# Kernel tuning notes

Measured on AMD Instinct MI355X. Metric: run time of the kernel, lower is better.

Reference implementation:

```python
import jax, jax.numpy as jnp
import numpy as np

G, N_REAL, C_IN, C_EDGE, H, D, C_EOUT = 4096, 31, 64, 64, 4, 64, 64
N_NODE = N_REAL + 1  # 32, last local node is the supernode


def setup_inputs() -> dict:
    key = jax.random.key(0)
    # per-graph edge template: bidirectional ring over real nodes (consecutive (u,v),(v,u) pairs),
    # then edges (u, supernode)
    u = np.arange(N_REAL)
    v = (u + 1) % N_REAL
    ring_src = np.stack([u, v], 1).reshape(-1)
    ring_dst = np.stack([v, u], 1).reshape(-1)
    ls = np.concatenate([ring_src, np.arange(N_REAL)])
    ld = np.concatenate([ring_dst, np.full(N_REAL, N_REAL)])
    Eg = ls.shape[0]  # 93
    off = np.arange(G) * N_NODE
    edge_index = np.stack([(off[:, None] + ls[None, :]).reshape(-1),
                           (off[:, None] + ld[None, :]).reshape(-1)])
    N = G * N_NODE
    E = G * Eg
    k1, k2, k3, k4, k5 = jax.random.split(key, 5)
    return {
        "x": jax.random.normal(k1, (N, C_IN), jnp.float32),
        "edge_index": jnp.asarray(edge_index, jnp.int32),
        "edge_inform": jax.random.normal(k2, (E, C_EDGE), jnp.float32) * 0.1,
        "batch": jnp.asarray(np.repeat(np.arange(G), N_NODE), jnp.int32),
        "edge_num": jnp.asarray(np.full(G, Eg), jnp.int32),
        "W_lin_l": jax.random.normal(k3, (C_IN + C_EDGE, H * D), jnp.float32) * 0.05,
        "att_l": jax.random.normal(k4, (1, H, D), jnp.float32) * 0.1,
        "bias": jnp.zeros((D,), jnp.float32),
        "W_ec": jax.random.normal(k5, (C_EDGE, C_EOUT), jnp.float32) * 0.1,
        "b_ec": jnp.zeros((C_EOUT,), jnp.float32),
    }


def reference(x, edge_index, edge_inform, batch, edge_num, W_lin_l, att_l, bias, W_ec, b_ec):
    # graph structure is static metadata -> numpy
    ei = np.asarray(edge_index)
    en = np.asarray(edge_num)
    N = x.shape[0]
    G_ = en.shape[0]
    Eg = int(en[0])
    n = N // G_
    src = jnp.asarray(ei[0])
    dst = jnp.asarray(ei[1])
    Hh, Dd = att_l.shape[1], att_l.shape[2]

    # degree counting (the per-edge python loop in the original)
    deg = jnp.zeros((N,), x.dtype).at[dst].add(1.0)

    # GAT-style edge attention + scatter-sum
    h = jnp.concatenate([x[src], edge_inform], axis=1) @ W_lin_l  # [E, H*D]
    h = h.reshape(-1, Hh, Dd)
    alpha = jax.nn.leaky_relu(jnp.sum(h * att_l, axis=-1))  # [E,H], slope 0.01
    amax = jax.ops.segment_max(alpha, dst, num_segments=N)
    ex = jnp.exp(alpha - amax[dst])
    a = ex / (jax.ops.segment_sum(ex, dst, num_segments=N)[dst] + 1e-16)
    xi = jax.ops.segment_sum(h * a[..., None], dst, num_segments=N)  # [N,H,D]
    out = xi.mean(axis=1) + bias

    # per-graph edge aggregation (structure uniform across graphs by construction)
    le = ei.reshape(2, G_, Eg) - (np.arange(G_) * n)[None, :, None]
    l0, l1 = le[0, 0], le[1, 0]  # local template indices, same for every graph
    midx = np.nonzero((l1 != n - 1) & (l0 != l1))[0]  # mask: drop supernode-dst & self-loops
    even = midx[0::2]
    C = edge_inform.shape[1]
    inf_g = edge_inform.reshape(G_, Eg, C)

    mdst = jnp.asarray(l1[midx])
    eisum = jax.vmap(lambda v: jax.ops.segment_sum(v, mdst, num_segments=n - 1))(inf_g[:, midx])  # [G,n-1,C]

    es, ed = l0[even], l1[even]
    deg_g = deg.reshape(G_, n)
    norm = deg_g[:, es] + deg_g[:, ed] - 2.0  # edge_norm; divide by edge_norm - 1
    temp = (eisum[:, es] + eisum[:, ed] - inf_g[:, even]) / (norm - 1.0)[..., None]  # [G,P,C]
    temps2 = jnp.repeat(temp, 2, axis=1)  # each temp appended twice

    l1_all = jnp.asarray(l1)
    cnt = jnp.zeros((n,), x.dtype).at[l1_all].add(1.0)
    esum_all = jax.vmap(lambda v: jax.ops.segment_sum(v, l1_all, num_segments=n))(inf_g)
    emean = esum_all / cnt[None, :, None]  # scatter reduce='mean'

    gather = jnp.concatenate([temps2, emean, emean[:, : n - 1]], axis=1).reshape(-1, C)
    new_edge_inform = jax.nn.leaky_relu(gather @ W_ec + b_ec)
    return out, new_edge_inform
```

## Files before the change

kernel.cpp:

```cpp
#include <hip/hip_runtime.h>
#include <hip/hip_fp16.h>

#define NUM_G 4096
#define RS 72
#define OUT2_OFF ((size_t)NUM_G * 32 * 64)

typedef _Float16 half8  __attribute__((ext_vector_type(8)));
typedef _Float16 half4v __attribute__((ext_vector_type(4)));
typedef _Float16 half2v __attribute__((ext_vector_type(2)));
typedef float    floatx4 __attribute__((ext_vector_type(4)));

__device__ __forceinline__ float lrelu(float v) { return v > 0.f ? v : 0.01f * v; }

__global__ void setup_prep(const float* __restrict__ W, const float* __restrict__ att,
                           const float* __restrict__ Wec,
                           _Float16* __restrict__ vp, _Float16* __restrict__ BT,
                           _Float16* __restrict__ BT2)
{
    const int t = threadIdx.x, b = blockIdx.x;
    if (b == 0) {
        for (int i = t; i < 512; i += 256) {
            const int h8 = i >> 6, k = i & 63;
            const int h = h8 & 3, ro = (h8 < 4) ? 0 : 64;
            float acc = 0.f;
            for (int d = 0; d < 64; ++d) acc += W[(ro + k) * 256 + h * 64 + d] * att[h * 64 + d];
            vp[i] = (_Float16)acc;
        }
    }
    for (int i = b * 4096 + t; i < (b + 1) * 4096; i += 256) {
        const int d = i >> 9, kk = i & 511, h = kk >> 7, k = kk & 127;
        BT[i] = (_Float16)W[k * 256 + h * 64 + d];
    }
    for (int i = b * 512 + t; i < b * 512 + 512; i += 256) {
        const int d = i >> 6, k = i & 63;
        BT2[i] = (_Float16)Wec[k * 64 + d];
    }
}

__global__ __launch_bounds__(256, 4) void fused_main(
    const float* __restrict__ x, const float* __restrict__ einf,
    const float* __restrict__ bias, const float* __restrict__ bec,
    const _Float16* __restrict__ vp, const _Float16* __restrict__ BT,
    const _Float16* __restrict__ BT2,
    float* __restrict__ out, float* __restrict__ out2)
{
    __shared__ __align__(16) _Float16 R[128 * RS];
    __shared__ __align__(16) unsigned char U[9216];
    _Float16* vpl  = (_Float16*)U;
    float*    sal  = (float*)(U + 1152);
    _Float16* virt = (_Float16*)(U + 5760);
    float*    al4  = (float*)(U + 6784);
    _Float16* A2   = (_Float16*)U;

    const int t = threadIdx.x;
    const int g = blockIdx.x;
    const int lane = t & 63;
    const int w = t >> 6;
    const int m16 = lane & 15, q = lane >> 4;

    {
        const float4* xg4 = (const float4*)(x + (size_t)g * 2048);
        for (int i = t; i < 512; i += 256) {
            float4 v = xg4[i];
            half4v h4 = {(_Float16)v.x, (_Float16)v.y, (_Float16)v.z, (_Float16)v.w};
            *(half4v*)(R + (i >> 4) * RS + (i & 15) * 4) = h4;
        }
        const float4* eg4 = (const float4*)(einf + (size_t)g * 5952);
        for (int i = t; i < 1488; i += 256) {
            float4 v = eg4[i];
            half4v h4 = {(_Float16)v.x, (_Float16)v.y, (_Float16)v.z, (_Float16)v.w};
            *(half4v*)(R + (32 + (i >> 4)) * RS + (i & 15) * 4) = h4;
        }
        for (int i = t; i < 512; i += 256)
            vpl[(i >> 6) * RS + (i & 63)] = vp[i];
    }
    __syncthreads();

    #pragma unroll
    for (int j = 0; j < 4; ++j) {
        const int combo = t + 256 * j;
        const int r = combo >> 3, h8 = combo & 7;
        const _Float16* rr = R + r * RS;
        const _Float16* vr = vpl + h8 * RS;
        half8 a8 = {0, 0, 0, 0, 0, 0, 0, 0};
        #pragma unroll
        for (int k8 = 0; k8 < 8; ++k8)
            a8 += (*(const half8*)(rr + k8 * 8)) * (*(const half8*)(vr + k8 * 8));
        float s = 0.f;
        #pragma unroll
        for (int jj = 0; jj < 8; ++jj) s += (float)a8[jj];
        sal[r * 9 + h8] = s;
    }
    __syncthreads();

    if (t < 128) {
        const int n = t >> 2, h = t & 3;
        if (n < 31) {
            const int s1 = (n + 30) % 31, s2 = (n + 1) % 31;
            const int e1 = 2 * s1, e2 = 2 * n + 1;
            const float a1 = lrelu(sal[s1 * 9 + h] + sal[(32 + e1) * 9 + 4 + h]);
            const float a2 = lrelu(sal[s2 * 9 + h] + sal[(32 + e2) * 9 + 4 + h]);
            const float m = fmaxf(a1, a2);
            const float x1 = __expf(a1 - m), x2 = __expf(a2 - m);
            const float inv = 1.f / (x1 + x2 + 1e-16f);
            al4[e1 * 4 + h] = x1 * inv;
            al4[e2 * 4 + h] = x2 * inv;
        } else {
            float m = -1e30f;
            for (int i = 0; i < 31; ++i)
                m = fmaxf(m, lrelu(sal[i * 9 + h] + sal[(94 + i) * 9 + 4 + h]));
            float sden = 1e-16f;
            for (int i = 0; i < 31; ++i)
                sden += __expf(lrelu(sal[i * 9 + h] + sal[(94 + i) * 9 + 4 + h]) - m);
            const float inv = 1.f / sden;
            for (int i = 0; i < 31; ++i)
                al4[(62 + i) * 4 + h] =
                    __expf(lrelu(sal[i * 9 + h] + sal[(94 + i) * 9 + 4 + h]) - m) * inv;
        }
    }
    __syncthreads();

    #pragma unroll
    for (int j = 0; j < 2; ++j) {
        const int c = t + 256 * j;
        const int h = c >> 7, hf = (c >> 6) & 1, k = c & 63;
        float acc = 0.f;
        for (int i = 0; i < 31; ++i)
            acc += al4[(62 + i) * 4 + h] * (float)R[(hf ? 94 + i : i) * RS + k];
        virt[c] = (_Float16)acc;
    }
    __syncthreads();

    {
        const int n0 = m16, n1 = 16 + m16;
        const int n1c = (n1 < 31) ? n1 : 30;
        const int s1_0 = (n0 + 30) % 31, s2_0 = (n0 + 1) % 31;
        const int e1_0 = 2 * s1_0, e2_0 = 2 * n0 + 1;
        const int s1_1 = (n1c + 30) % 31, s2_1 = (n1c + 1) % 31;
        const int e1_1 = 2 * s1_1, e2_1 = 2 * n1c + 1;
        _Float16 a1_0[4], a2_0[4], a1_1[4], a2_1[4];
        #pragma unroll
        for (int h = 0; h < 4; ++h) {
            a1_0[h] = (_Float16)al4[e1_0 * 4 + h];
            a2_0[h] = (_Float16)al4[e2_0 * 4 + h];
            a1_1[h] = (_Float16)al4[e1_1 * 4 + h];
            a2_1[h] = (_Float16)al4[e2_1 * 4 + h];
        }
        const int co = w * 16 + m16;
        floatx4 acc0 = {0.f, 0.f, 0.f, 0.f}, acc1 = {0.f, 0.f, 0.f, 0.f};
        #pragma unroll
        for (int kk = 0; kk < 16; ++kk) {
            const int h = kk >> 2, hf = (kk >> 1) & 1;
            const int k0 = (kk & 1) * 32 + q * 8;
            const int r1_0 = hf ? 32 + e1_0 : s1_0, r2_0 = hf ? 32 + e2_0 : s2_0;
            const int r1_1 = hf ? 32 + e1_1 : s1_1, r2_1 = hf ? 32 + e2_1 : s2_1;
            half8 b = *(const half8*)(BT + co * 512 + kk * 32 + q * 8);
            half8 x1 = *(const half8*)(R + r1_0 * RS + k0);
            half8 x2 = *(const half8*)(R + r2_0 * RS + k0);
            half8 af0 = x1 * a1_0[h] + x2 * a2_0[h];
            acc0 = __builtin_amdgcn_mfma_f32_16x16x32_f16(af0, b, acc0, 0, 0, 0);
            half8 y1 = *(const half8*)(R + r1_1 * RS + k0);
            half8 y2 = *(const half8*)(R + r2_1 * RS + k0);
            half8 af1 = y1 * a1_1[h] + y2 * a2_1[h];
            half8 vv = *(const half8*)(virt + kk * 32 + q * 8);
            af1 = (m16 == 15) ? vv : af1;
            acc1 = __builtin_amdgcn_mfma_f32_16x16x32_f16(af1, b, acc1, 0, 0, 0);
        }
        const float bv = bias[co];
        float* og = out + (size_t)g * 2048;
        #pragma unroll
        for (int r = 0; r < 4; ++r) {
            og[(q * 4 + r) * 64 + co]        = 0.25f * acc0[r] + bv;
            og[(16 + q * 4 + r) * 64 + co]   = 0.25f * acc1[r] + bv;
        }
    }

    half8 b2a = *(const half8*)(BT2 + (w * 16 + m16) * 64 + 0 * 32 + q * 8);
    half8 b2b = *(const half8*)(BT2 + (w * 16 + m16) * 64 + 1 * 32 + q * 8);
    __syncthreads();

    {
        const _Float16* E = R + 32 * RS;
        for (int idx = t; idx < 62 * 32; idx += 256) {
            const int r = idx >> 5, k = (idx & 31) * 2;
            half2v v;
            if (r < 31) {
                const int ra = 2 * ((r + 30) % 31), rb = 2 * r + 1, rc = 2 * ((r + 1) % 31) + 1;
                v = *(const half2v*)(E + ra * RS + k) + *(const half2v*)(E + rb * RS + k)
                  + *(const half2v*)(E + rc * RS + k);
            } else {
                const int jj = r - 31;
                const int ra = 2 * ((jj + 30) % 31), rb = 2 * jj + 1;
                v = (*(const half2v*)(E + ra * RS + k) + *(const half2v*)(E + rb * RS + k))
                    * (_Float16)0.5f;
            }
            *(half2v*)(A2 + r * RS + k) = v;
        }
        if (t < 64) {
            float s = 0.f;
            for (int i = 0; i < 31; ++i) s += (float)E[(62 + i) * RS + t];
            A2[62 * RS + t] = (_Float16)(s * (1.f / 31.f));
        } else if (t < 128) {
            A2[63 * RS + (t - 64)] = (_Float16)0.f;
        }
    }
    __syncthreads();

    {
        floatx4 z = {0.f, 0.f, 0.f, 0.f};
        floatx4 acc2[4]; acc2[0] = z; acc2[1] = z; acc2[2] = z; acc2[3] = z;
        #pragma unroll
        for (int kk = 0; kk < 2; ++kk) {
            half8 b = kk ? b2b : b2a;
            #pragma unroll
            for (int mt = 0; mt < 4; ++mt) {
                half8 a = *(const half8*)(A2 + (mt * 16 + m16) * RS + kk * 32 + q * 8);
                acc2[mt] = __builtin_amdgcn_mfma_f32_16x16x32_f16(a, b, acc2[mt], 0, 0, 0);
            }
        }
        const int co = w * 16 + m16;
        const float bv2 = bec[co];
        float* o2 = out2 + (size_t)g * 8000;
        #pragma unroll
        for (int mt = 0; mt < 4; ++mt) {
            #pragma unroll
            for (int r = 0; r < 4; ++r) {
                const int row = mt * 16 + q * 4 + r;
                if (row >= 63) continue;
                const float v = lrelu(acc2[mt][r] + bv2);
                if (row < 31) {
                    o2[(2 * row) * 64 + co]     = v;
                    o2[(2 * row + 1) * 64 + co] = v;
                } else if (row < 62) {
                    o2[(62 + row - 31) * 64 + co] = v;
                    o2[(94 + row - 31) * 64 + co] = v;
                } else {
                    o2[93 * 64 + co] = v;
                }
            }
        }
    }
}

extern "C" void kernel_launch(void* const* d_in, const int* in_sizes, int n_in,
                              void* d_out, int out_size, void* d_ws, size_t ws_size,
                              hipStream_t stream) {
    const float* x    = (const float*)d_in[0];
    const float* einf = (const float*)d_in[2];
    const float* W    = (const float*)d_in[5];
    const float* att  = (const float*)d_in[6];
    const float* bias = (const float*)d_in[7];
    const float* Wec  = (const float*)d_in[8];
    const float* bec  = (const float*)d_in[9];
    float* out  = (float*)d_out;
    float* out2 = out + OUT2_OFF;

    _Float16* vp  = (_Float16*)d_ws;
    _Float16* BT  = (_Float16*)((char*)d_ws + 1024);
    _Float16* BT2 = (_Float16*)((char*)d_ws + 1024 + 65536);

    setup_prep<<<8, 256, 0, stream>>>(W, att, Wec, vp, BT, BT2);
    fused_main<<<NUM_G, 256, 0, stream>>>(x, einf, bias, bec, vp, BT, BT2, out, out2);
}
```

Baseline: 324.2 us.

## Double block to 512 threads, use MFMA for attention scores and virtual node

The per-graph block grows to 512 threads (8 waves). Attention logits and the supernode aggregation move from scalar dot products onto MFMA. The edge-feature aggregation for the second GEMM now overlaps with the softmax phase on otherwise idle threads, and A2 gets its own shared buffer so a barrier can be dropped. The main GEMM work is split so each wave handles one row tile instead of two. The risks are higher shared-memory use and more register pressure under launch_bounds(512,8), which could cut occupancy, and more waves sitting idle during the serial softmax phase.

```diff
diff --git a/kernel.cpp b/kernel.cpp
--- a/kernel.cpp
+++ b/kernel.cpp
@@ -7,24 +7,25 @@
 
 typedef _Float16 half8  __attribute__((ext_vector_type(8)));
 typedef _Float16 half4v __attribute__((ext_vector_type(4)));
-typedef _Float16 half2v __attribute__((ext_vector_type(2)));
 typedef float    floatx4 __attribute__((ext_vector_type(4)));
 
 __device__ __forceinline__ float lrelu(float v) { return v > 0.f ? v : 0.01f * v; }
 
 __global__ void setup_prep(const float* __restrict__ W, const float* __restrict__ att,
                            const float* __restrict__ Wec,
-                           _Float16* __restrict__ vp, _Float16* __restrict__ BT,
+                           _Float16* __restrict__ vp16, _Float16* __restrict__ BT,
                            _Float16* __restrict__ BT2)
 {
     const int t = threadIdx.x, b = blockIdx.x;
     if (b == 0) {
-        for (int i = t; i < 512; i += 256) {
+        for (int i = t; i < 1024; i += 256) {
             const int h8 = i >> 6, k = i & 63;
-            const int h = h8 & 3, ro = (h8 < 4) ? 0 : 64;
             float acc = 0.f;
-            for (int d = 0; d < 64; ++d) acc += W[(ro + k) * 256 + h * 64 + d] * att[h * 64 + d];
-            vp[i] = (_Float16)acc;
+            if (h8 < 8) {
+                const int h = h8 & 3, ro = (h8 < 4) ? 0 : 64;
+                for (int d = 0; d < 64; ++d) acc += W[(ro + k) * 256 + h * 64 + d] * att[h * 64 + d];
+            }
+            vp16[i] = (_Float16)acc;
         }
     }
     for (int i = b * 4096 + t; i < (b + 1) * 4096; i += 256) {
@@ -37,20 +38,18 @@
     }
 }
 
-__global__ __launch_bounds__(256, 4) void fused_main(
+__global__ __launch_bounds__(512, 8) void fused_main(
     const float* __restrict__ x, const float* __restrict__ einf,
     const float* __restrict__ bias, const float* __restrict__ bec,
-    const _Float16* __restrict__ vp, const _Float16* __restrict__ BT,
+    const _Float16* __restrict__ vp16, const _Float16* __restrict__ BT,
     const _Float16* __restrict__ BT2,
     float* __restrict__ out, float* __restrict__ out2)
 {
     __shared__ __align__(16) _Float16 R[128 * RS];
-    __shared__ __align__(16) unsigned char U[9216];
-    _Float16* vpl  = (_Float16*)U;
-    float*    sal  = (float*)(U + 1152);
-    _Float16* virt = (_Float16*)(U + 5760);
-    float*    al4  = (float*)(U + 6784);
-    _Float16* A2   = (_Float16*)U;
+    __shared__ __align__(16) _Float16 A2[64 * RS];
+    __shared__ __align__(16) float    sal[128 * 9];
+    __shared__ __align__(16) float    al4[93 * 4];
+    __shared__ __align__(16) _Float16 virt[512];
 
     const int t = threadIdx.x;
     const int g = blockIdx.x;
@@ -60,36 +59,38 @@
 
     {
         const float4* xg4 = (const float4*)(x + (size_t)g * 2048);
-        for (int i = t; i < 512; i += 256) {
-            float4 v = xg4[i];
+        {
+            float4 v = xg4[t];
             half4v h4 = {(_Float16)v.x, (_Float16)v.y, (_Float16)v.z, (_Float16)v.w};
-            *(half4v*)(R + (i >> 4) * RS + (i & 15) * 4) = h4;
+            *(half4v*)(R + (t >> 4) * RS + (t & 15) * 4) = h4;
         }
         const float4* eg4 = (const float4*)(einf + (size_t)g * 5952);
-        for (int i = t; i < 1488; i += 256) {
+        for (int i = t; i < 1488; i += 512) {
             float4 v = eg4[i];
             half4v h4 = {(_Float16)v.x, (_Float16)v.y, (_Float16)v.z, (_Float16)v.w};
             *(half4v*)(R + (32 + (i >> 4)) * RS + (i & 15) * 4) = h4;
         }
-        for (int i = t; i < 512; i += 256)
-            vpl[(i >> 6) * RS + (i & 63)] = vp[i];
-    }
-    __syncthreads();
-
-    #pragma unroll
-    for (int j = 0; j < 4; ++j) {
-        const int combo = t + 256 * j;
-        const int r = combo >> 3, h8 = combo & 7;
-        const _Float16* rr = R + r * RS;
-        const _Float16* vr = vpl + h8 * RS;
-        half8 a8 = {0, 0, 0, 0, 0, 0, 0, 0};
-        #pragma unroll
-        for (int k8 = 0; k8 < 8; ++k8)
-            a8 += (*(const half8*)(rr + k8 * 8)) * (*(const half8*)(vr + k8 * 8));
-        float s = 0.f;
-        #pragma unroll
-        for (int jj = 0; jj < 8; ++jj) s += (float)a8[jj];
-        sal[r * 9 + h8] = s;
+        if (t < 27) {
+            half8 z = {0, 0, 0, 0, 0, 0, 0, 0};
+            *(half8*)(R + 125 * RS + t * 8) = z;
+        }
+    }
+    __syncthreads();
+
+    {
+        const _Float16* arow = R + (w * 16 + m16) * RS;
+        floatx4 s = {0.f, 0.f, 0.f, 0.f};
+        #pragma unroll
+        for (int kc = 0; kc < 2; ++kc) {
+            half8 aF = *(const half8*)(arow + kc * 32 + q * 8);
+            half8 bF = *(const half8*)(vp16 + m16 * 64 + kc * 32 + q * 8);
+            s = __builtin_amdgcn_mfma_f32_16x16x32_f16(aF, bF, s, 0, 0, 0);
+        }
+        if (m16 < 8) {
+            #pragma unroll
+            for (int r = 0; r < 4; ++r)
+                sal[(w * 16 + q * 4 + r) * 9 + m16] = s[r];
+        }
     }
     __syncthreads();
 
@@ -117,117 +118,121 @@
                 al4[(62 + i) * 4 + h] =
                     __expf(lrelu(sal[i * 9 + h] + sal[(94 + i) * 9 + 4 + h]) - m) * inv;
         }
-    }
-    __syncthreads();
-
-    #pragma unroll
-    for (int j = 0; j < 2; ++j) {
-        const int c = t + 256 * j;
-        const int h = c >> 7, hf = (c >> 6) & 1, k = c & 63;
-        float acc = 0.f;
-        for (int i = 0; i < 31; ++i)
-            acc += al4[(62 + i) * 4 + h] * (float)R[(hf ? 94 + i : i) * RS + k];
-        virt[c] = (_Float16)acc;
-    }
-    __syncthreads();
-
-    {
-        const int n0 = m16, n1 = 16 + m16;
-        const int n1c = (n1 < 31) ? n1 : 30;
-        const int s1_0 = (n0 + 30) % 31, s2_0 = (n0 + 1) % 31;
-        const int e1_0 = 2 * s1_0, e2_0 = 2 * n0 + 1;
-        const int s1_1 = (n1c + 30) % 31, s2_1 = (n1c + 1) % 31;
-        const int e1_1 = 2 * s1_1, e2_1 = 2 * n1c + 1;
-        _Float16 a1_0[4], a2_0[4], a1_1[4], a2_1[4];
-        #pragma unroll
-        for (int h = 0; h < 4; ++h) {
-            a1_0[h] = (_Float16)al4[e1_0 * 4 + h];
-            a2_0[h] = (_Float16)al4[e2_0 * 4 + h];
-            a1_1[h] = (_Float16)al4[e1_1 * 4 + h];
-            a2_1[h] = (_Float16)al4[e2_1 * 4 + h];
-        }
-        const int co = w * 16 + m16;
-        floatx4 acc0 = {0.f, 0.f, 0.f, 0.f}, acc1 = {0.f, 0.f, 0.f, 0.f};
-        #pragma unroll
-        for (int kk = 0; kk < 16; ++kk) {
-            const int h = kk >> 2, hf = (kk >> 1) & 1;
-            const int k0 = (kk & 1) * 32 + q * 8;
-            const int r1_0 = hf ? 32 + e1_0 : s1_0, r2_0 = hf ? 32 + e2_0 : s2_0;
-            const int r1_1 = hf ? 32 + e1_1 : s1_1, r2_1 = hf ? 32 + e2_1 : s2_1;
-            half8 b = *(const half8*)(BT + co * 512 + kk * 32 + q * 8);
-            half8 x1 = *(const half8*)(R + r1_0 * RS + k0);
-            half8 x2 = *(const half8*)(R + r2_0 * RS + k0);
-            half8 af0 = x1 * a1_0[h] + x2 * a2_0[h];
-            acc0 = __builtin_amdgcn_mfma_f32_16x16x32_f16(af0, b, acc0, 0, 0, 0);
-            half8 y1 = *(const half8*)(R + r1_1 * RS + k0);
-            half8 y2 = *(const half8*)(R + r2_1 * RS + k0);
-            half8 af1 = y1 * a1_1[h] + y2 * a2_1[h];
-            half8 vv = *(const half8*)(virt + kk * 32 + q * 8);
-            af1 = (m16 == 15) ? vv : af1;
-            acc1 = __builtin_amdgcn_mfma_f32_16x16x32_f16(af1, b, acc1, 0, 0, 0);
-        }
-        const float bv = bias[co];
-        float* og = out + (size_t)g * 2048;
-        #pragma unroll
-        for (int r = 0; r < 4; ++r) {
-            og[(q * 4 + r) * 64 + co]        = 0.25f * acc0[r] + bv;
-            og[(16 + q * 4 + r) * 64 + co]   = 0.25f * acc1[r] + bv;
-        }
-    }
-
-    half8 b2a = *(const half8*)(BT2 + (w * 16 + m16) * 64 + 0 * 32 + q * 8);
-    half8 b2b = *(const half8*)(BT2 + (w * 16 + m16) * 64 + 1 * 32 + q * 8);
-    __syncthreads();
-
-    {
+    } else {
         const _Float16* E = R + 32 * RS;
-        for (int idx = t; idx < 62 * 32; idx += 256) {
-            const int r = idx >> 5, k = (idx & 31) * 2;
-            half2v v;
+        for (int idx = t - 128; idx < 992; idx += 384) {
+            const int r = idx >> 4, c = (idx & 15) * 4;
+            half4v v;
             if (r < 31) {
                 const int ra = 2 * ((r + 30) % 31), rb = 2 * r + 1, rc = 2 * ((r + 1) % 31) + 1;
-                v = *(const half2v*)(E + ra * RS + k) + *(const half2v*)(E + rb * RS + k)
-                  + *(const half2v*)(E + rc * RS + k);
+                v = *(const half4v*)(E + ra * RS + c) + *(const half4v*)(E + rb * RS + c)
+                  + *(const half4v*)(E + rc * RS + c);
             } else {
                 const int jj = r - 31;
                 const int ra = 2 * ((jj + 30) % 31), rb = 2 * jj + 1;
-                v = (*(const half2v*)(E + ra * RS + k) + *(const half2v*)(E + rb * RS + k))
+                v = (*(const half4v*)(E + ra * RS + c) + *(const half4v*)(E + rb * RS + c))
                     * (_Float16)0.5f;
             }
-            *(half2v*)(A2 + r * RS + k) = v;
-        }
-        if (t < 64) {
+            *(half4v*)(A2 + r * RS + c) = v;
+        }
+        if (t < 192) {
+            const int c = t - 128;
             float s = 0.f;
-            for (int i = 0; i < 31; ++i) s += (float)E[(62 + i) * RS + t];
-            A2[62 * RS + t] = (_Float16)(s * (1.f / 31.f));
-        } else if (t < 128) {
-            A2[63 * RS + (t - 64)] = (_Float16)0.f;
-        }
-    }
-    __syncthreads();
-
-    {
+            for (int i = 0; i < 31; ++i) s += (float)E[(62 + i) * RS + c];
+            A2[62 * RS + c] = (_Float16)(s * (1.f / 31.f));
+        } else if (t < 256) {
+            A2[63 * RS + (t - 192)] = (_Float16)0.f;
+        }
+    }
+    __syncthreads();
+
+    {
+        const int hf = w >> 2, nt = w & 3;
+        const int base = hf ? 94 : 0;
+        half8 aV, bV;
+        #pragma unroll
+        for (int j = 0; j < 8; ++j) {
+            const int i = q * 8 + j;
+            aV[j] = (m16 < 4 && i < 31) ? (_Float16)al4[(62 + i) * 4 + m16] : (_Float16)0.f;
+            bV[j] = (i < 31) ? R[(base + i) * RS + nt * 16 + m16] : (_Float16)0.f;
+        }
+        floatx4 vc = {0.f, 0.f, 0.f, 0.f};
+        vc = __builtin_amdgcn_mfma_f32_16x16x32_f16(aV, bV, vc, 0, 0, 0);
+        if (q == 0) {
+            #pragma unroll
+            for (int r = 0; r < 4; ++r)
+                virt[r * 128 + hf * 64 + nt * 16 + m16] = (_Float16)vc[r];
+        }
+    }
+    __syncthreads();
+
+    const int ti = w >> 2, cg = w & 3;
+    const int co = cg * 16 + m16;
+
+    {
+        const int n = ti * 16 + m16;
+        const int nc = (n < 31) ? n : 30;
+        const int s1 = (nc + 30) % 31, s2 = (nc + 1) % 31;
+        const int e1 = 2 * s1, e2 = 2 * nc + 1;
+        _Float16 a1[4], a2[4];
+        #pragma unroll
+        for (int h = 0; h < 4; ++h) {
+            a1[h] = (_Float16)al4[e1 * 4 + h];
+            a2[h] = (_Float16)al4[e2 * 4 + h];
+        }
+        floatx4 acc = {0.f, 0.f, 0.f, 0.f};
+        #pragma unroll
+        for (int hf = 0; hf < 2; ++hf) {
+            const int rA = hf ? 32 + e1 : s1;
+            const int rB = hf ? 32 + e2 : s2;
+            #pragma unroll
+            for (int kc = 0; kc < 2; ++kc) {
+                const int k0 = kc * 32 + q * 8;
+                half8 xa = *(const half8*)(R + rA * RS + k0);
+                half8 xb = *(const half8*)(R + rB * RS + k0);
+                #pragma unroll
+                for (int h = 0; h < 4; ++h) {
+                    half8 b = *(const half8*)(BT + co * 512 + (h * 4 + hf * 2 + kc) * 32 + q * 8);
+                    half8 af = xa * a1[h] + xb * a2[h];
+                    if (ti == 1) {
+                        half8 vv = *(const half8*)(virt + h * 128 + hf * 64 + k0);
+                        af = (m16 == 15) ? vv : af;
+                    }
+                    acc = __builtin_amdgcn_mfma_f32_16x16x32_f16(af, b, acc, 0, 0, 0);
+                }
+            }
+        }
+        const float bv = bias[co];
+        float* og = out + (size_t)g * 2048;
+        #pragma unroll
+        for (int r = 0; r < 4; ++r)
+            og[(ti * 16 + q * 4 + r) * 64 + co] = 0.25f * acc[r] + bv;
+    }
+
+    {
+        half8 b2a = *(const half8*)(BT2 + co * 64 + q * 8);
+        half8 b2b = *(const half8*)(BT2 + co * 64 + 32 + q * 8);
+        const int mt0 = ti * 2;
         floatx4 z = {0.f, 0.f, 0.f, 0.f};
-        floatx4 acc2[4]; acc2[0] = z; acc2[1] = z; acc2[2] = z; acc2[3] = z;
+        floatx4 acc2[2]; acc2[0] = z; acc2[1] = z;
         #pragma unroll
         for (int kk = 0; kk < 2; ++kk) {
             half8 b = kk ? b2b : b2a;
             #pragma unroll
-            for (int mt = 0; mt < 4; ++mt) {
-                half8 a = *(const half8*)(A2 + (mt * 16 + m16) * RS + kk * 32 + q * 8);
-                acc2[mt] = __builtin_amdgcn_mfma_f32_16x16x32_f16(a, b, acc2[mt], 0, 0, 0);
-            }
-        }
-        const int co = w * 16 + m16;
+            for (int m = 0; m < 2; ++m) {
+                half8 a = *(const half8*)(A2 + ((mt0 + m) * 16 + m16) * RS + kk * 32 + q * 8);
+                acc2[m] = __builtin_amdgcn_mfma_f32_16x16x32_f16(a, b, acc2[m], 0, 0, 0);
+            }
+        }
         const float bv2 = bec[co];
         float* o2 = out2 + (size_t)g * 8000;
         #pragma unroll
-        for (int mt = 0; mt < 4; ++mt) {
+        for (int m = 0; m < 2; ++m) {
             #pragma unroll
             for (int r = 0; r < 4; ++r) {
-                const int row = mt * 16 + q * 4 + r;
+                const int row = (mt0 + m) * 16 + q * 4 + r;
                 if (row >= 63) continue;
-                const float v = lrelu(acc2[mt][r] + bv2);
+                const float v = lrelu(acc2[m][r] + bv2);
                 if (row < 31) {
                     o2[(2 * row) * 64 + co]     = v;
                     o2[(2 * row + 1) * 64 + co] = v;
@@ -255,10 +260,10 @@
     float* out  = (float*)d_out;
     float* out2 = out + OUT2_OFF;
 
-    _Float16* vp  = (_Float16*)d_ws;
-    _Float16* BT  = (_Float16*)((char*)d_ws + 1024);
-    _Float16* BT2 = (_Float16*)((char*)d_ws + 1024 + 65536);
-
-    setup_prep<<<8, 256, 0, stream>>>(W, att, Wec, vp, BT, BT2);
-    fused_main<<<NUM_G, 256, 0, stream>>>(x, einf, bias, bec, vp, BT, BT2, out, out2);
+    _Float16* vp16 = (_Float16*)d_ws;
+    _Float16* BT   = (_Float16*)((char*)d_ws + 2048);
+    _Float16* BT2  = (_Float16*)((char*)d_ws + 2048 + 65536);
+
+    setup_prep<<<8, 256, 0, stream>>>(W, att, Wec, vp16, BT, BT2);
+    fused_main<<<NUM_G, 512, 0, stream>>>(x, einf, bias, bec, vp16, BT, BT2, out, out2);
 }
```

New measurement: 352.2 us. +8.7%, slower.
